# Kernel optimization log

Measured on AMD Instinct MI355X. Metric: run time of the kernel, lower is better.

Reference implementation:

```python
import jax, jax.numpy as jnp
import numpy as np

M, NM, EM = 7, 1024, 32768        # modules, nodes/module, edges/module
N, E = M * NM, M * EM
F, D, H = 128, 64, 4              # node feats, hidden_channels, heads
HC = H * D


def setup_inputs() -> dict:
    key = jax.random.key(0)
    ks = jax.random.split(key, 20)
    x = jax.random.normal(ks[0], (N, F), jnp.float32)
    # intra-module edges; nodes of module m occupy [m*NM, (m+1)*NM)
    base = jnp.repeat(jnp.arange(M, dtype=jnp.int32) * NM, EM)
    src = base + jax.random.randint(ks[1], (E,), 0, NM, dtype=jnp.int32)
    dst = base + jax.random.randint(ks[2], (E,), 0, NM, dtype=jnp.int32)
    edge_index = jnp.stack([src, dst])
    module_assignments = jnp.repeat(jnp.arange(M, dtype=jnp.int32), NM)
    rn = lambda k, sh: jax.random.normal(k, sh, jnp.float32) * 0.05
    return dict(
        x=x, edge_index=edge_index, module_assignments=module_assignments,
        g1_w=rn(ks[3], (M, F, H, D)), g1_as=rn(ks[4], (M, H, D)), g1_ad=rn(ks[5], (M, H, D)),
        g1_b=jnp.zeros((M, HC), jnp.float32),
        g2_w=rn(ks[6], (M, HC, 1, D)), g2_as=rn(ks[7], (M, 1, D)), g2_ad=rn(ks[8], (M, 1, D)),
        g2_b=jnp.zeros((M, D), jnp.float32),
        sa_in_w=rn(ks[9], (M, 3 * D, D)), sa_in_b=jnp.zeros((M, 3 * D), jnp.float32),
        sa_out_w=rn(ks[10], (M, D, D)), sa_out_b=jnp.zeros((M, D), jnp.float32),
        ca_in_w=rn(ks[11], (3 * D, D)), ca_in_b=jnp.zeros((3 * D,), jnp.float32),
        ca_out_w=rn(ks[12], (D, D)), ca_out_b=jnp.zeros((D,), jnp.float32),
        fusion_w=jnp.ones((M,), jnp.float32) / M,
        fc_w=rn(ks[13], (M * D, D)), fc_b=jnp.zeros((D,), jnp.float32),
        c1_w=rn(ks[14], (D, D // 2)), c1_b=jnp.zeros((D // 2,), jnp.float32),
        c2_w=rn(ks[15], (D // 2, 2)), c2_b=jnp.zeros((2,), jnp.float32))


def _gat(x, src, dst, W, a_s, a_d, b, concat):
    # PyG-style GATConv (eval mode, add_self_loops=True). x:[NM,Fin], W:[Fin,h,c]
    h = jnp.einsum('nf,fhc->nhc', x, W)          # [NM,h,c]
    es = (h * a_s).sum(-1)                        # [NM,h]
    ed = (h * a_d).sum(-1)
    sl = jnp.arange(NM, dtype=src.dtype)
    s = jnp.concatenate([src, sl])                # add self-loops
    d = jnp.concatenate([dst, sl])
    e = jax.nn.leaky_relu(es[s] + ed[d], 0.2)     # [E+NM,h]
    mx = jax.ops.segment_max(e, d, num_segments=NM)
    ex = jnp.exp(e - mx[d])
    den = jax.ops.segment_sum(ex, d, num_segments=NM)
    alpha = ex / (den[d] + 1e-16)
    out = jax.ops.segment_sum(alpha[:, :, None] * h[s], d, num_segments=NM)  # [NM,h,c]
    out = out.reshape(NM, -1) if concat else out.mean(axis=1)
    return out + b


def _mha(x, in_w, in_b, out_w, out_b, nh):
    # torch nn.MultiheadAttention, batch_first, batch=1, eval mode
    L, d = x.shape
    dh = d // nh
    q, k, v = jnp.split(x @ in_w.T + in_b, 3, axis=-1)
    q = q.reshape(L, nh, dh); k = k.reshape(L, nh, dh); v = v.reshape(L, nh, dh)
    att = jax.nn.softmax(jnp.einsum('qhd,khd->hqk', q, k) * (1.0 / np.sqrt(dh)), axis=-1)
    o = jnp.einsum('hqk,khd->qhd', att, v).reshape(L, d)
    return o @ out_w.T + out_b


def _forward(x, edge_index, g1_w, g1_as, g1_ad, g1_b, g2_w, g2_as, g2_ad, g2_b,
             sa_in_w, sa_in_b, sa_out_w, sa_out_b, ca_in_w, ca_in_b, ca_out_w, ca_out_b,
             fusion_w, fc_w, fc_b, c1_w, c1_b, c2_w, c2_b):
    # per-module subgraph extraction + reindex: modules are contiguous node
    # blocks and edges are grouped per module, so mask/relabel is a reshape.
    ei = edge_index.reshape(2, M, EM)
    offs = (jnp.arange(M, dtype=ei.dtype) * NM)[:, None]
    src = ei[0] - offs                 # [M,EM] local indices
    dst = ei[1] - offs
    xm = x.reshape(M, NM, F)

    def per_module(xm_, s_, d_, g1w, g1a, g1d, g1b_, g2w_, g2a, g2d, g2b_, siw, sib, sow, sob):
        h = jax.nn.relu(_gat(xm_, s_, d_, g1w, g1a, g1d, g1b_, True))   # [NM,HC]
        h = jax.nn.relu(_gat(h, s_, d_, g2w_, g2a, g2d, g2b_, False))   # [NM,D]
        h = _mha(h, siw, sib, sow, sob, H)                              # module self-attention
        return h.mean(axis=0)                                            # [D]

    reps = jax.vmap(per_module)(xm, src, dst, g1_w, g1_as, g1_ad, g1_b,
                                g2_w, g2_as, g2_ad, g2_b,
                                sa_in_w, sa_in_b, sa_out_w, sa_out_b)    # [M,D]
    cross = _mha(reps, ca_in_w, ca_in_b, ca_out_w, ca_out_b, H)          # [M,D]
    w = jax.nn.softmax(fusion_w)
    fused = (cross * w[:, None]).reshape(1, M * D) @ fc_w + fc_b         # [1,D]
    out = jax.nn.relu(fused @ c1_w + c1_b) @ c2_w + c2_b                 # [1,2]
    return out, reps


def reference(x, edge_index, module_assignments, g1_w, g1_as, g1_ad, g1_b,
              g2_w, g2_as, g2_ad, g2_b, sa_in_w, sa_in_b, sa_out_w, sa_out_b,
              ca_in_w, ca_in_b, ca_out_w, ca_out_b, fusion_w, fc_w, fc_b,
              c1_w, c1_b, c2_w, c2_b):
    del module_assignments  # encoded as contiguous blocks of NM nodes per module
    return _forward(x, edge_index, g1_w, g1_as, g1_ad, g1_b, g2_w, g2_as, g2_ad, g2_b,
                    sa_in_w, sa_in_b, sa_out_w, sa_out_b, ca_in_w, ca_in_b, ca_out_w,
                    ca_out_b, fusion_w, fc_w, fc_b, c1_w, c1_b, c2_w, c2_b)
```

## Files before the change

### kernel.cpp

```cpp
#include <hip/hip_runtime.h>
#include <hip/hip_bf16.h>
#include <stdint.h>

#define MODS 7
#define NMOD 1024
#define EMOD 32768
#define NN (MODS*NMOD)
#define EE (MODS*EMOD)
#define KC2 4
#define G1B (MODS*16*4)

typedef __hip_bfloat16 bf16;

static __device__ __forceinline__ float lrelu(float x){ return x > 0.f ? x : 0.2f*x; }
static __device__ __forceinline__ float bfu(unsigned short u){ return __uint_as_float(((unsigned)u) << 16); }
static __device__ __forceinline__ float2 f2fma(float2 a, float2 b, float2 c){
  return make_float2(fmaf(a.x,b.x,c.x), fmaf(a.y,b.y,c.y));
}

template<int K, int JT, bool TB, int RT, bool OBF, int SC, bool TRQ>
__device__ __forceinline__ void gemm_body(int b, const float* __restrict__ A,
    const float* __restrict__ B, const float* __restrict__ bias, void* __restrict__ Cv,
    const float* __restrict__ a_s, const float* __restrict__ a_d,
    float* __restrict__ es, float* __restrict__ ed) {
  constexpr int jt = JT/64;
  constexpr int rtiles = NMOD/RT;
  constexpr int RPT = RT/16;
  int ct = b % jt; b /= jt;
  int rt = b % rtiles; b /= rtiles;
  int m = b;
  int row0 = m*NMOD + rt*RT;
  int col0 = ct*64;
  __shared__ float Ast[32][RT+4];
  __shared__ float Bs[32][68];
  float acc[RPT][4] = {};
  int tid = threadIdx.x;
  int tr = (tid >> 4) * RPT;
  int tc = (tid & 15) * 4;
  const float* Bm = B + (size_t)m*K*JT;
  for (int k0 = 0; k0 < K; k0 += 32) {
    if constexpr (RT >= 32) {
      constexpr int ANUM = RT*32/1024;
      #pragma unroll
      for (int i = 0; i < ANUM; ++i) {
        int it = tid + i*256;
        int rr = it >> 3, kk0 = (it & 7)*4;
        float4 t = *(const float4*)&A[(size_t)(row0+rr)*K + k0 + kk0];
        Ast[kk0+0][rr] = t.x; Ast[kk0+1][rr] = t.y; Ast[kk0+2][rr] = t.z; Ast[kk0+3][rr] = t.w;
      }
    } else {
      if (tid < 128) {
        int rr = tid >> 3, kk0 = (tid & 7)*4;
        float4 t = *(const float4*)&A[(size_t)(row0+rr)*K + k0 + kk0];
        Ast[kk0+0][rr] = t.x; Ast[kk0+1][rr] = t.y; Ast[kk0+2][rr] = t.z; Ast[kk0+3][rr] = t.w;
      }
    }
    #pragma unroll
    for (int i = 0; i < 2; ++i) {
      int it = tid + i*256;
      if (!TB) {
        int kk = it >> 4, jj0 = (it & 15)*4;
        float4 t = *(const float4*)&Bm[(size_t)(k0+kk)*JT + col0 + jj0];
        Bs[kk][jj0] = t.x; Bs[kk][jj0+1] = t.y; Bs[kk][jj0+2] = t.z; Bs[kk][jj0+3] = t.w;
      } else {
        int jj = it >> 3, kk0 = (it & 7)*4;
        float4 t = *(const float4*)&Bm[(size_t)(col0+jj)*K + k0 + kk0];
        Bs[kk0+0][jj] = t.x; Bs[kk0+1][jj] = t.y; Bs[kk0+2][jj] = t.z; Bs[kk0+3][jj] = t.w;
      }
    }
    __syncthreads();
    #pragma unroll
    for (int kk = 0; kk < 32; ++kk) {
      float4 bv = *(const float4*)&Bs[kk][tc];
      float av[RPT];
      if constexpr (RPT == 4) {
        float4 t = *(const float4*)&Ast[kk][tr];
        av[0] = t.x; av[1] = t.y; av[2] = t.z; av[3] = t.w;
      } else if constexpr (RPT == 2) {
        av[0] = Ast[kk][tr]; av[1] = Ast[kk][tr+1];
      } else {
        av[0] = Ast[kk][tr];
      }
      #pragma unroll
      for (int i = 0; i < RPT; ++i) {
        acc[i][0] += av[i]*bv.x; acc[i][1] += av[i]*bv.y;
        acc[i][2] += av[i]*bv.z; acc[i][3] += av[i]*bv.w;
      }
    }
    __syncthreads();
  }
  float4 bb = {0,0,0,0};
  if (bias) bb = *(const float4*)&bias[m*JT + col0 + tc];
  #pragma unroll
  for (int i = 0; i < RPT; ++i) {
    float4 o = { acc[i][0]+bb.x, acc[i][1]+bb.y, acc[i][2]+bb.z, acc[i][3]+bb.w };
    if constexpr (TRQ) {
      float* Cp = (float*)Cv;
      size_t idx = ((size_t)(m*3 + ct)*NMOD + (rt*RT + tr + i))*64 + tc;
      *(float4*)&Cp[idx] = o;
    } else {
      size_t idx = (size_t)(row0+tr+i)*JT + col0 + tc;
      if constexpr (OBF) {
        bf16* Cp = (bf16*)Cv;
        bf16 tmp[4] = { __float2bfloat16(o.x), __float2bfloat16(o.y),
                        __float2bfloat16(o.z), __float2bfloat16(o.w) };
        *(uint2*)&Cp[idx] = *(const uint2*)tmp;
      } else {
        float* Cp = (float*)Cv;
        *(float4*)&Cp[idx] = o;
      }
    }
  }
  if constexpr (SC == 4) {
    int hh = ct;
    float4 as4 = *(const float4*)&a_s[(m*4 + hh)*64 + tc];
    float4 ad4 = *(const float4*)&a_d[(m*4 + hh)*64 + tc];
    #pragma unroll
    for (int i = 0; i < RPT; ++i) {
      float s = acc[i][0]*as4.x + acc[i][1]*as4.y + acc[i][2]*as4.z + acc[i][3]*as4.w;
      float d = acc[i][0]*ad4.x + acc[i][1]*ad4.y + acc[i][2]*ad4.z + acc[i][3]*ad4.w;
      #pragma unroll
      for (int off = 1; off < 16; off <<= 1) { s += __shfl_xor(s, off); d += __shfl_xor(d, off); }
      if ((tid & 15) == 0) {
        es[(row0+tr+i)*4 + hh] = s;
        ed[(row0+tr+i)*4 + hh] = d;
      }
    }
  }
  if constexpr (SC == 1) {
    float4 as4 = *(const float4*)&a_s[m*64 + tc];
    float4 ad4 = *(const float4*)&a_d[m*64 + tc];
    float s = acc[0][0]*as4.x + acc[0][1]*as4.y + acc[0][2]*as4.z + acc[0][3]*as4.w;
    float d = acc[0][0]*ad4.x + acc[0][1]*ad4.y + acc[0][2]*ad4.z + acc[0][3]*ad4.w;
    #pragma unroll
    for (int off = 1; off < 16; off <<= 1) { s += __shfl_xor(s, off); d += __shfl_xor(d, off); }
    if ((tid & 15) == 0) { es[row0+tr] = s; ed[row0+tr] = d; }
  }
}

__device__ __forceinline__ void hist_body(int mm, const int* __restrict__ dst,
                                          int* __restrict__ rs, int* __restrict__ rs2) {
  __shared__ int hc[NMOD];
  __shared__ int hws[4];
  int tid = threadIdx.x;
  hc[tid] = 0; hc[tid+256] = 0; hc[tid+512] = 0; hc[tid+768] = 0;
  __syncthreads();
  const int4* d4 = (const int4*)(dst + mm*EMOD);
  int base = mm*NMOD;
  for (int it = tid; it < EMOD/4; it += 256) {
    int4 d = d4[it];
    atomicAdd(&hc[d.x - base], 1); atomicAdd(&hc[d.y - base], 1);
    atomicAdd(&hc[d.z - base], 1); atomicAdd(&hc[d.w - base], 1);
  }
  __syncthreads();
  int lane = tid & 63, wid = tid >> 6;
  int i0 = tid*4;
  int v0 = hc[i0], v1 = hc[i0+1], v2 = hc[i0+2], v3 = hc[i0+3];
  int T = v0+v1+v2+v3;
  int X = T;
  #pragma unroll
  for (int off = 1; off < 64; off <<= 1) { int t = __shfl_up(X, off); if (lane >= off) X += t; }
  if (lane == 63) hws[wid] = X;
  __syncthreads();
  int woff = 0;
  #pragma unroll
  for (int w = 0; w < 4; ++w) if (w < wid) woff += hws[w];
  int ex = mm*EMOD + woff + X - T;
  int4 o = make_int4(ex, ex+v0, ex+v0+v1, ex+v0+v1+v2);
  *(int4*)&rs[base + i0]  = o;
  *(int4*)&rs2[base + i0] = o;
  if (mm == MODS-1 && tid == 255) rs[NN] = EE;
}

__global__ __launch_bounds__(256) void k_g1h(const float* __restrict__ x,
    const float* __restrict__ g1w, bf16* __restrict__ h1,
    const float* __restrict__ a_s, const float* __restrict__ a_d,
    float* __restrict__ es, float* __restrict__ ed,
    const int* __restrict__ dst, int* __restrict__ rs, int* __restrict__ rs2) {
  if (blockIdx.x < G1B)
    gemm_body<128,256,false,64,true,4,false>(blockIdx.x, x, g1w, nullptr, h1, a_s, a_d, es, ed);
  else
    hist_body(blockIdx.x - G1B, dst, rs, rs2);
}

__global__ __launch_bounds__(256) void k_g2s(const float* __restrict__ A,
    const float* __restrict__ B, bf16* __restrict__ h2,
    const float* __restrict__ a_s, const float* __restrict__ a_d,
    float* __restrict__ es, float* __restrict__ ed) {
  gemm_body<256,64,false,16,true,1,false>(blockIdx.x, A, B, nullptr, h2, a_s, a_d, es, ed);
}

__global__ __launch_bounds__(256) void k_gqkv(const float* __restrict__ A,
    const float* __restrict__ B, const float* __restrict__ bias, float* __restrict__ C) {
  gemm_body<64,192,true,64,false,0,true>(blockIdx.x, A, B, bias, C, nullptr, nullptr, nullptr, nullptr);
}

__global__ void k_fill(const int* __restrict__ src, const int* __restrict__ dst,
                       int* __restrict__ rs2, int* __restrict__ csr_src) {
  int e = blockIdx.x*256 + threadIdx.x;
  if (e < EE) {
    int pos = atomicAdd(&rs2[dst[e]], 1);
    csr_src[pos] = src[e];
  }
}

__global__ __launch_bounds__(256) void k_agg4(const bf16* __restrict__ h,
    const float* __restrict__ es, const float* __restrict__ ed, const int* __restrict__ rs,
    const int* __restrict__ csr_src, const float* __restrict__ bias, float* __restrict__ out) {
  int wid = __builtin_amdgcn_readfirstlane(threadIdx.x >> 6);
  int n = blockIdx.x*4 + wid;
  int lane = threadIdx.x & 63;
  int hh = lane >> 4;
  int m = n >> 10;
  const unsigned short* hp = (const unsigned short*)h;
  float edv = ed[n*4 + hh];
  float p0 = __expf(lrelu(es[n*4 + hh] + edv));
  float den = p0;
  ushort4 v0 = *(const ushort4*)&hp[(size_t)n*256 + lane*4];
  float a0 = p0*bfu(v0.x), a1 = p0*bfu(v0.y), a2 = p0*bfu(v0.z), a3 = p0*bfu(v0.w);
  int beg = rs[n], end = rs[n+1];
  int i = beg;
  for (; i + 8 <= end; i += 8) {
    int ss[8]; ushort4 ww[8]; float qq[8];
    #pragma unroll
    for (int k = 0; k < 8; ++k) ss[k] = csr_src[i+k];
    #pragma unroll
    for (int k = 0; k < 8; ++k) ww[k] = *(const ushort4*)&hp[(size_t)ss[k]*256 + lane*4];
    #pragma unroll
    for (int k = 0; k < 8; ++k) qq[k] = __expf(lrelu(es[ss[k]*4 + hh] + edv));
    #pragma unroll
    for (int k = 0; k < 8; ++k) {
      den += qq[k];
      a0 += qq[k]*bfu(ww[k].x); a1 += qq[k]*bfu(ww[k].y);
      a2 += qq[k]*bfu(ww[k].z); a3 += qq[k]*bfu(ww[k].w);
    }
  }
  for (; i < end; ++i) {
    int s = csr_src[i];
    ushort4 w = *(const ushort4*)&hp[(size_t)s*256 + lane*4];
    float q = __expf(lrelu(es[s*4 + hh] + edv));
    den += q;
    a0 += q*bfu(w.x); a1 += q*bfu(w.y); a2 += q*bfu(w.z); a3 += q*bfu(w.w);
  }
  float inv = 1.f/den;
  float4 bb = *(const float4*)&bias[m*256 + lane*4];
  float4 o = { fmaxf(a0*inv + bb.x, 0.f), fmaxf(a1*inv + bb.y, 0.f),
               fmaxf(a2*inv + bb.z, 0.f), fmaxf(a3*inv + bb.w, 0.f) };
  *(float4*)&out[(size_t)n*256 + lane*4] = o;
}

__global__ __launch_bounds__(256) void k_agg1(const bf16* __restrict__ h,
    const float* __restrict__ es, const float* __restrict__ ed, const int* __restrict__ rs,
    const int* __restrict__ csr_src, const float* __restrict__ bias, float* __restrict__ out) {
  int wid = __builtin_amdgcn_readfirstlane(threadIdx.x >> 6);
  int n = blockIdx.x*4 + wid;
  int lane = threadIdx.x & 63;
  int m = n >> 10;
  float edv = ed[n];
  float p0 = __expf(lrelu(es[n] + edv));
  float den = p0;
  float acc = p0 * __bfloat162float(h[(size_t)n*64 + lane]);
  int beg = rs[n], end = rs[n+1];
  int i = beg;
  for (; i + 8 <= end; i += 8) {
    int ss[8]; float vv[8]; float qq[8];
    #pragma unroll
    for (int k = 0; k < 8; ++k) ss[k] = csr_src[i+k];
    #pragma unroll
    for (int k = 0; k < 8; ++k) vv[k] = __bfloat162float(h[(size_t)ss[k]*64 + lane]);
    #pragma unroll
    for (int k = 0; k < 8; ++k) qq[k] = __expf(lrelu(es[ss[k]] + edv));
    #pragma unroll
    for (int k = 0; k < 8; ++k) { den += qq[k]; acc += qq[k]*vv[k]; }
  }
  for (; i < end; ++i) {
    int s = csr_src[i];
    float q = __expf(lrelu(es[s] + edv));
    den += q;
    acc += q * __bfloat162float(h[(size_t)s*64 + lane]);
  }
  float v = acc/den + bias[m*64 + lane];
  out[(size_t)n*64 + lane] = fmaxf(v, 0.f);
}

__global__ __launch_bounds__(256) void k_attn(const float* __restrict__ qkv,
    float* __restrict__ pd, float* __restrict__ pacc) {
  int b = blockIdx.x;
  int kcg = b & (KC2-1); b /= KC2;
  int h = b & 3; b >>= 2;
  int qt = b & 15; int m = b >> 4;
  int lane = threadIdx.x & 63;
  int wu = __builtin_amdgcn_readfirstlane(threadIdx.x >> 6);
  int nl = qt*64 + lane;
  int n = m*NMOD + nl;
  float2 q2[8];
  const float* qrow = qkv + ((size_t)(m*3 + 0)*NMOD + nl)*64 + h*16;
  #pragma unroll
  for (int c = 0; c < 8; ++c) {
    float2 t = *(const float2*)(qrow + 2*c);
    q2[c] = make_float2(t.x*0.25f, t.y*0.25f);
  }
  int k0 = kcg*256 + wu*64;
  const float* kb = qkv + ((size_t)(m*3 + 1)*NMOD + k0)*64 + h*16;
  const float* vb = qkv + ((size_t)(m*3 + 2)*NMOD + k0)*64 + h*16;
  float den = 0.f;
  float2 acc2[8] = {};
  float2 kreg[8];
  #pragma unroll
  for (int c = 0; c < 8; ++c) kreg[c] = ((const float2*)kb)[c];
  for (int j = 0; j < 64; ++j) {
    const float2* nk = (const float2*)(kb + (size_t)(j+1)*64);
    float2 knx[8];
    #pragma unroll
    for (int c = 0; c < 8; ++c) knx[c] = nk[c];
    float2 d0 = {0,0}, d1 = {0,0};
    #pragma unroll
    for (int c = 0; c < 8; c += 2) { d0 = f2fma(q2[c], kreg[c], d0); d1 = f2fma(q2[c+1], kreg[c+1], d1); }
    float p = __expf((d0.x + d0.y) + (d1.x + d1.y));
    den += p;
    const float2* vr2 = (const float2*)(vb + (size_t)j*64);
    float2 pp = {p, p};
    #pragma unroll
    for (int c = 0; c < 8; ++c) acc2[c] = f2fma(pp, vr2[c], acc2[c]);
    #pragma unroll
    for (int c = 0; c < 8; ++c) kreg[c] = knx[c];
  }
  __shared__ float red[4][64][17];
  #pragma unroll
  for (int c = 0; c < 8; ++c) { red[wu][lane][2*c] = acc2[c].x; red[wu][lane][2*c+1] = acc2[c].y; }
  red[wu][lane][16] = den;
  __syncthreads();
  if (wu == 0) {
    size_t o = ((size_t)n*4 + h)*KC2 + kcg;
    pd[o] = red[0][lane][16] + red[1][lane][16] + red[2][lane][16] + red[3][lane][16];
    #pragma unroll
    for (int c = 0; c < 16; ++c)
      pacc[o*16 + c] = red[0][lane][c] + red[1][lane][c] + red[2][lane][c] + red[3][lane][c];
  }
}

__global__ __launch_bounds__(256) void k_comb(const float* __restrict__ pd,
    const float* __restrict__ pacc, float* __restrict__ partial) {
  int m = blockIdx.x >> 4, chunk = blockIdx.x & 15;
  __shared__ float part[4][64];
  int tid = threadIdx.x;
  int j = tid & 63, pp = tid >> 6;
  int h = j >> 4, c = j & 15;
  float s = 0.f;
  int base = m*NMOD + chunk*64;
  #pragma unroll 4
  for (int i = pp*16; i < pp*16 + 16; ++i) {
    int n = base + i;
    size_t o = ((size_t)n*4 + h)*KC2;
    float den = pd[o] + pd[o+1] + pd[o+2] + pd[o+3];
    float t = pacc[o*16 + c] + pacc[(o+1)*16 + c] + pacc[(o+2)*16 + c] + pacc[(o+3)*16 + c];
    s += t/den;
  }
  part[pp][j] = s;
  __syncthreads();
  if (pp == 0) partial[(size_t)blockIdx.x*64 + j] = part[0][j]+part[1][j]+part[2][j]+part[3][j];
}

__global__ void k_reps2(const float* __restrict__ partial, const float* __restrict__ out_w,
                        const float* __restrict__ out_b, float* __restrict__ reps,
                        float* __restrict__ dout) {
  int m = blockIdx.x;
  __shared__ float abar[64];
  int tid = threadIdx.x;
  if (tid < 64) {
    float s = 0.f;
    #pragma unroll
    for (int k = 0; k < 16; ++k) s += partial[(size_t)(m*16 + k)*64 + tid];
    abar[tid] = s * (1.f/NMOD);
  }
  __syncthreads();
  if (tid < 64) {
    float r = out_b[m*64 + tid];
    const float* wr = out_w + (size_t)m*64*64 + (size_t)tid*64;
    #pragma unroll
    for (int k = 0; k < 64; ++k) r += abar[k]*wr[k];
    reps[m*64 + tid] = r;
    dout[2 + m*64 + tid] = r;
  }
}

__global__ __launch_bounds__(256) void k_final(const float* __restrict__ reps,
    const float* __restrict__ ca_in_w, const float* __restrict__ ca_in_b,
    const float* __restrict__ ca_out_w, const float* __restrict__ ca_out_b,
    const float* __restrict__ fusion_w, const float* __restrict__ fc_w,
    const float* __restrict__ fc_b, const float* __restrict__ c1_w,
    const float* __restrict__ c1_b, const float* __restrict__ c2_w,
    const float* __restrict__ c2_b, float* __restrict__ dout) {
  __shared__ float R[7][64];
  __shared__ float QKV[7][192];
  __shared__ float SC[4][7][8];
  __shared__ float AL[4][7][8];
  __shared__ float O[7][64];
  __shared__ float CR[7][64];
  __shared__ float W[8];
  __shared__ float part[4][64];
  __shared__ float FU[64];
  __shared__ float HM[32];
  int tid = threadIdx.x, lane = tid & 63;
  for (int i = tid; i < 448; i += 256) R[i>>6][i&63] = reps[i];
  __syncthreads();
  {
    int sub = tid & 3, tt0 = tid >> 2;
    #pragma unroll 3
    for (int it = 0; it < 21; ++it) {
      int t = tt0 + it*64;
      int r = t/192, j = t - r*192;
      const float4* wr = (const float4*)&ca_in_w[j*64 + sub*16];
      const float4* rr = (const float4*)&R[r][sub*16];
      float s = 0.f;
      #pragma unroll
      for (int c = 0; c < 4; ++c) {
        float4 a = rr[c], w4 = wr[c];
        s += a.x*w4.x + a.y*w4.y + a.z*w4.z + a.w*w4.w;
      }
      s += __shfl_xor(s, 1); s += __shfl_xor(s, 2);
      if (sub == 0) QKV[r][j] = s + ca_in_b[j];
    }
    if (tid == 252) {
      float p[7]; float den = 0.f;
      #pragma unroll
      for (int i = 0; i < 7; ++i) { p[i] = __expf(fusion_w[i]); den += p[i]; }
      float inv = 1.f/den;
      #pragma unroll
      for (int i = 0; i < 7; ++i) W[i] = p[i]*inv;
    }
  }
  __syncthreads();
  if (tid < 196) {
    int hh = tid/49, rem = tid - hh*49, qi = rem/7, ki = rem - qi*7;
    float s = 0.f;
    #pragma unroll
    for (int c = 0; c < 16; ++c) s += QKV[qi][hh*16 + c]*QKV[ki][64 + hh*16 + c];
    SC[hh][qi][ki] = __expf(s*0.25f);
  }
  __syncthreads();
  if (tid < 28) {
    int hh = tid/7, qi = tid - hh*7;
    float den = 0.f;
    #pragma unroll
    for (int k = 0; k < 7; ++k) den += SC[hh][qi][k];
    float inv = 1.f/den;
    #pragma unroll
    for (int k = 0; k < 7; ++k) AL[hh][qi][k] = SC[hh][qi][k]*inv;
  }
  __syncthreads();
  for (int i = tid; i < 448; i += 256) {
    int qi = i >> 6, j = i & 63, hh = j >> 4;
    float s = 0.f;
    #pragma unroll
    for (int k = 0; k < 7; ++k) s += AL[hh][qi][k]*QKV[k][128 + j];
    O[qi][j] = s;
  }
  __syncthreads();
  {
    int sub = tid & 3, tt0 = tid >> 2;
    #pragma unroll
    for (int it = 0; it < 7; ++it) {
      int t = tt0 + it*64;
      int qi = t >> 6, j = t & 63;
      const float4* wr = (const float4*)&ca_out_w[j*64 + sub*16];
      const float4* orow = (const float4*)&O[qi][sub*16];
      float s = 0.f;
      #pragma unroll
      for (int c = 0; c < 4; ++c) {
        float4 a = orow[c], w4 = wr[c];
        s += a.x*w4.x + a.y*w4.y + a.z*w4.z + a.w*w4.w;
      }
      s += __shfl_xor(s, 1); s += __shfl_xor(s, 2);
      if (sub == 0) CR[qi][j] = s + ca_out_b[j];
    }
  }
  __syncthreads();
  {
    int w = tid >> 6;
    float s = 0.f;
    #pragma unroll 4
    for (int i = w*112; i < w*112 + 112; ++i)
      s += CR[i>>6][i&63]*W[i>>6]*fc_w[(size_t)i*64 + lane];
    part[w][lane] = s;
  }
  __syncthreads();
  if (tid < 64) FU[tid] = part[0][tid] + part[1][tid] + part[2][tid] + part[3][tid] + fc_b[tid];
  __syncthreads();
  if (tid < 128) {
    int sub = tid & 3, j = tid >> 2;
    float s = 0.f;
    #pragma unroll
    for (int c = 0; c < 16; ++c) { int k = sub*16 + c; s += FU[k]*c1_w[k*32 + j]; }
    s += __shfl_xor(s, 1); s += __shfl_xor(s, 2);
    if (sub == 0) HM[j] = fmaxf(s + c1_b[j], 0.f);
  }
  __syncthreads();
  if (tid < 2) {
    float s = c2_b[tid];
    #pragma unroll
    for (int k = 0; k < 32; ++k) s += HM[k]*c2_w[k*2 + tid];
    dout[tid] = s;
  }
}

extern "C" void kernel_launch(void* const* d_in, const int* in_sizes, int n_in,
                              void* d_out, int out_size, void* d_ws, size_t ws_size,
                              hipStream_t stream) {
  (void)in_sizes; (void)n_in; (void)out_size; (void)ws_size;
  const float* x       = (const float*)d_in[0];
  const int*   ei      = (const int*)d_in[1];
  const float* g1_w    = (const float*)d_in[3];
  const float* g1_as   = (const float*)d_in[4];
  const float* g1_ad   = (const float*)d_in[5];
  const float* g1_b    = (const float*)d_in[6];
  const float* g2_w    = (const float*)d_in[7];
  const float* g2_as   = (const float*)d_in[8];
  const float* g2_ad   = (const float*)d_in[9];
  const float* g2_b    = (const float*)d_in[10];
  const float* sa_in_w = (const float*)d_in[11];
  const float* sa_in_b = (const float*)d_in[12];
  const float* sa_out_w= (const float*)d_in[13];
  const float* sa_out_b= (const float*)d_in[14];
  const float* ca_in_w = (const float*)d_in[15];
  const float* ca_in_b = (const float*)d_in[16];
  const float* ca_out_w= (const float*)d_in[17];
  const float* ca_out_b= (const float*)d_in[18];
  const float* fusion_w= (const float*)d_in[19];
  const float* fc_w    = (const float*)d_in[20];
  const float* fc_b    = (const float*)d_in[21];
  const float* c1_w    = (const float*)d_in[22];
  const float* c1_b    = (const float*)d_in[23];
  const float* c2_w    = (const float*)d_in[24];
  const float* c2_b    = (const float*)d_in[25];
  float* dout = (float*)d_out;

  const int* src = ei;
  const int* dst = ei + EE;

  char* p = (char*)d_ws;
  int* rs      = (int*)p; p += (size_t)(NN+4)*sizeof(int);
  int* rs2     = (int*)p; p += (size_t)(NN+4)*sizeof(int);
  int* csr_src = (int*)p; p += (size_t)EE*sizeof(int);
  p = (char*)(((uintptr_t)p + 255) & ~(uintptr_t)255);
  float* h1f  = (float*)p; p += (size_t)NN*256*4;
  float* es1  = (float*)p; p += (size_t)NN*4*4;
  float* ed1  = (float*)p; p += (size_t)NN*4*4;
  float* gat1 = (float*)p; p += (size_t)NN*256*4;
  float* h2f  = (float*)p; p += (size_t)NN*64*4;
  float* es2  = (float*)p; p += (size_t)NN*4;
  float* ed2  = (float*)p; p += (size_t)NN*4;
  float* z    = (float*)p; p += (size_t)NN*64*4;
  float* partial = (float*)p; p += (size_t)112*64*4;
  float* reps = (float*)p; p += (size_t)MODS*64*4;
  bf16* h1    = (bf16*)h1f;
  bf16* h2    = (bf16*)h2f;
  float* qkv  = h1f;
  float* pacc = gat1;
  float* pd   = h2f;

  k_g1h<<<G1B + MODS, 256, 0, stream>>>(x, g1_w, h1, g1_as, g1_ad, es1, ed1, dst, rs, rs2);
  k_fill<<<(EE+255)/256, 256, 0, stream>>>(src, dst, rs2, csr_src);
  k_agg4<<<NN/4, 256, 0, stream>>>(h1, es1, ed1, rs, csr_src, g1_b, gat1);
  k_g2s<<<MODS*64, 256, 0, stream>>>(gat1, g2_w, h2, g2_as, g2_ad, es2, ed2);
  k_agg1<<<NN/4, 256, 0, stream>>>(h2, es2, ed2, rs, csr_src, g2_b, z);
  k_gqkv<<<MODS*16*3, 256, 0, stream>>>(z, sa_in_w, sa_in_b, qkv);
  k_attn<<<MODS*16*4*KC2, 256, 0, stream>>>(qkv, pd, pacc);
  k_comb<<<112, 256, 0, stream>>>(pd, pacc, partial);
  k_reps2<<<MODS, 256, 0, stream>>>(partial, sa_out_w, sa_out_b, reps, dout);
  k_final<<<1, 256, 0, stream>>>(reps, ca_in_w, ca_in_b, ca_out_w, ca_out_b,
                                 fusion_w, fc_w, fc_b, c1_w, c1_b, c2_w, c2_b, dout);
}
```

Baseline: 141.9 us.

## Halve GEMM row tiles, vectorize CSR fill, fold reps projection into final kernel

Halves the row tile of the layer-1 and QKV GEMMs and doubles their grid sizes for more parallelism. The CSR fill now handles four edges per thread with int4 loads. The combine stage is split into 32 chunks per module. The separate reps kernel is removed and its mean and out-projection are folded into the single-block final kernel, saving one launch. The trade-off is more per-block overhead from smaller tiles and more serial work inside the one-block final kernel.

```diff
diff --git a/kernel.cpp b/kernel.cpp
--- a/kernel.cpp
+++ b/kernel.cpp
@@ -8,7 +8,8 @@
 #define NN (MODS*NMOD)
 #define EE (MODS*EMOD)
 #define KC2 4
-#define G1B (MODS*16*4)
+#define G1B (MODS*32*4)
+#define NCHUNK 32
 
 typedef __hip_bfloat16 bf16;
 
@@ -178,7 +179,7 @@
     float* __restrict__ es, float* __restrict__ ed,
     const int* __restrict__ dst, int* __restrict__ rs, int* __restrict__ rs2) {
   if (blockIdx.x < G1B)
-    gemm_body<128,256,false,64,true,4,false>(blockIdx.x, x, g1w, nullptr, h1, a_s, a_d, es, ed);
+    gemm_body<128,256,false,32,true,4,false>(blockIdx.x, x, g1w, nullptr, h1, a_s, a_d, es, ed);
   else
     hist_body(blockIdx.x - G1B, dst, rs, rs2);
 }
@@ -192,15 +193,19 @@
 
 __global__ __launch_bounds__(256) void k_gqkv(const float* __restrict__ A,
     const float* __restrict__ B, const float* __restrict__ bias, float* __restrict__ C) {
-  gemm_body<64,192,true,64,false,0,true>(blockIdx.x, A, B, bias, C, nullptr, nullptr, nullptr, nullptr);
+  gemm_body<64,192,true,32,false,0,true>(blockIdx.x, A, B, bias, C, nullptr, nullptr, nullptr, nullptr);
 }
 
 __global__ void k_fill(const int* __restrict__ src, const int* __restrict__ dst,
                        int* __restrict__ rs2, int* __restrict__ csr_src) {
-  int e = blockIdx.x*256 + threadIdx.x;
-  if (e < EE) {
-    int pos = atomicAdd(&rs2[dst[e]], 1);
-    csr_src[pos] = src[e];
+  int e4 = blockIdx.x*256 + threadIdx.x;
+  if (e4 < EE/4) {
+    int4 s = ((const int4*)src)[e4];
+    int4 d = ((const int4*)dst)[e4];
+    csr_src[atomicAdd(&rs2[d.x], 1)] = s.x;
+    csr_src[atomicAdd(&rs2[d.y], 1)] = s.y;
+    csr_src[atomicAdd(&rs2[d.z], 1)] = s.z;
+    csr_src[atomicAdd(&rs2[d.w], 1)] = s.w;
   }
 }
 
@@ -296,9 +301,10 @@
   float2 q2[8];
   const float* qrow = qkv + ((size_t)(m*3 + 0)*NMOD + nl)*64 + h*16;
   #pragma unroll
-  for (int c = 0; c < 8; ++c) {
-    float2 t = *(const float2*)(qrow + 2*c);
-    q2[c] = make_float2(t.x*0.25f, t.y*0.25f);
+  for (int c = 0; c < 4; ++c) {
+    float4 t = *(const float4*)(qrow + 4*c);
+    q2[2*c]   = make_float2(t.x*0.25f, t.y*0.25f);
+    q2[2*c+1] = make_float2(t.z*0.25f, t.w*0.25f);
   }
   int k0 = kcg*256 + wu*64;
   const float* kb = qkv + ((size_t)(m*3 + 1)*NMOD + k0)*64 + h*16;
@@ -341,15 +347,15 @@
 
 __global__ __launch_bounds__(256) void k_comb(const float* __restrict__ pd,
     const float* __restrict__ pacc, float* __restrict__ partial) {
-  int m = blockIdx.x >> 4, chunk = blockIdx.x & 15;
+  int m = blockIdx.x >> 5, chunk = blockIdx.x & 31;
   __shared__ float part[4][64];
   int tid = threadIdx.x;
   int j = tid & 63, pp = tid >> 6;
   int h = j >> 4, c = j & 15;
   float s = 0.f;
-  int base = m*NMOD + chunk*64;
+  int base = m*NMOD + chunk*32;
   #pragma unroll 4
-  for (int i = pp*16; i < pp*16 + 16; ++i) {
+  for (int i = pp*8; i < pp*8 + 8; ++i) {
     int n = base + i;
     size_t o = ((size_t)n*4 + h)*KC2;
     float den = pd[o] + pd[o+1] + pd[o+2] + pd[o+3];
@@ -361,36 +367,15 @@
   if (pp == 0) partial[(size_t)blockIdx.x*64 + j] = part[0][j]+part[1][j]+part[2][j]+part[3][j];
 }
 
-__global__ void k_reps2(const float* __restrict__ partial, const float* __restrict__ out_w,
-                        const float* __restrict__ out_b, float* __restrict__ reps,
-                        float* __restrict__ dout) {
-  int m = blockIdx.x;
-  __shared__ float abar[64];
-  int tid = threadIdx.x;
-  if (tid < 64) {
-    float s = 0.f;
-    #pragma unroll
-    for (int k = 0; k < 16; ++k) s += partial[(size_t)(m*16 + k)*64 + tid];
-    abar[tid] = s * (1.f/NMOD);
-  }
-  __syncthreads();
-  if (tid < 64) {
-    float r = out_b[m*64 + tid];
-    const float* wr = out_w + (size_t)m*64*64 + (size_t)tid*64;
-    #pragma unroll
-    for (int k = 0; k < 64; ++k) r += abar[k]*wr[k];
-    reps[m*64 + tid] = r;
-    dout[2 + m*64 + tid] = r;
-  }
-}
-
-__global__ __launch_bounds__(256) void k_final(const float* __restrict__ reps,
+__global__ __launch_bounds__(256) void k_final(const float* __restrict__ partial,
+    const float* __restrict__ out_w, const float* __restrict__ out_b,
     const float* __restrict__ ca_in_w, const float* __restrict__ ca_in_b,
     const float* __restrict__ ca_out_w, const float* __restrict__ ca_out_b,
     const float* __restrict__ fusion_w, const float* __restrict__ fc_w,
     const float* __restrict__ fc_b, const float* __restrict__ c1_w,
     const float* __restrict__ c1_b, const float* __restrict__ c2_w,
     const float* __restrict__ c2_b, float* __restrict__ dout) {
+  __shared__ float PR[7][64];
   __shared__ float R[7][64];
   __shared__ float QKV[7][192];
   __shared__ float SC[4][7][8];
@@ -402,7 +387,38 @@
   __shared__ float FU[64];
   __shared__ float HM[32];
   int tid = threadIdx.x, lane = tid & 63;
-  for (int i = tid; i < 448; i += 256) R[i>>6][i&63] = reps[i];
+  {
+    int j = tid & 63, g = tid >> 6;
+    for (int m = g; m < 7; m += 4) {
+      float s = 0.f;
+      #pragma unroll
+      for (int k = 0; k < NCHUNK; ++k) s += partial[(size_t)(m*NCHUNK + k)*64 + j];
+      PR[m][j] = s * (1.f/NMOD);
+    }
+  }
+  __syncthreads();
+  {
+    int sub = tid & 3, tt0 = tid >> 2;
+    #pragma unroll
+    for (int it = 0; it < 7; ++it) {
+      int t = tt0 + it*64;
+      int qi = t >> 6, j = t & 63;
+      const float4* wr = (const float4*)&out_w[((size_t)qi*64 + j)*64 + sub*16];
+      const float4* rr = (const float4*)&PR[qi][sub*16];
+      float s = 0.f;
+      #pragma unroll
+      for (int c = 0; c < 4; ++c) {
+        float4 a = rr[c], w4 = wr[c];
+        s += a.x*w4.x + a.y*w4.y + a.z*w4.z + a.w*w4.w;
+      }
+      s += __shfl_xor(s, 1); s += __shfl_xor(s, 2);
+      if (sub == 0) {
+        float r = s + out_b[qi*64 + j];
+        R[qi][j] = r;
+        dout[2 + qi*64 + j] = r;
+      }
+    }
+  }
   __syncthreads();
   {
     int sub = tid & 3, tt0 = tid >> 2;
@@ -551,8 +567,7 @@
   float* es2  = (float*)p; p += (size_t)NN*4;
   float* ed2  = (float*)p; p += (size_t)NN*4;
   float* z    = (float*)p; p += (size_t)NN*64*4;
-  float* partial = (float*)p; p += (size_t)112*64*4;
-  float* reps = (float*)p; p += (size_t)MODS*64*4;
+  float* partial = (float*)p; p += (size_t)MODS*NCHUNK*64*4;
   bf16* h1    = (bf16*)h1f;
   bf16* h2    = (bf16*)h2f;
   float* qkv  = h1f;
@@ -560,14 +575,14 @@
   float* pd   = h2f;
 
   k_g1h<<<G1B + MODS, 256, 0, stream>>>(x, g1_w, h1, g1_as, g1_ad, es1, ed1, dst, rs, rs2);
-  k_fill<<<(EE+255)/256, 256, 0, stream>>>(src, dst, rs2, csr_src);
+  k_fill<<<(EE/4+255)/256, 256, 0, stream>>>(src, dst, rs2, csr_src);
   k_agg4<<<NN/4, 256, 0, stream>>>(h1, es1, ed1, rs, csr_src, g1_b, gat1);
   k_g2s<<<MODS*64, 256, 0, stream>>>(gat1, g2_w, h2, g2_as, g2_ad, es2, ed2);
   k_agg1<<<NN/4, 256, 0, stream>>>(h2, es2, ed2, rs, csr_src, g2_b, z);
-  k_gqkv<<<MODS*16*3, 256, 0, stream>>>(z, sa_in_w, sa_in_b, qkv);
+  k_gqkv<<<MODS*32*3, 256, 0, stream>>>(z, sa_in_w, sa_in_b, qkv);
   k_attn<<<MODS*16*4*KC2, 256, 0, stream>>>(qkv, pd, pacc);
-  k_comb<<<112, 256, 0, stream>>>(pd, pacc, partial);
-  k_reps2<<<MODS, 256, 0, stream>>>(partial, sa_out_w, sa_out_b, reps, dout);
-  k_final<<<1, 256, 0, stream>>>(reps, ca_in_w, ca_in_b, ca_out_w, ca_out_b,
+  k_comb<<<MODS*NCHUNK, 256, 0, stream>>>(pd, pacc, partial);
+  k_final<<<1, 256, 0, stream>>>(partial, sa_out_w, sa_out_b,
+                                 ca_in_w, ca_in_b, ca_out_w, ca_out_b,
                                  fusion_w, fc_w, fc_b, c1_w, c1_b, c2_w, c2_b, dout);
 }
```

Result: slower. 144.9 us (+2.1%).
